# Performance work log

Hardware: AMD Instinct MI355X
Metric: run time of the kernel (lower is better)

The kernel has to match this reference:

```python
import jax, jax.numpy as jnp
import numpy as np

D_MODEL = 1024
N_HEADS = 16
HEAD_DIM = D_MODEL // N_HEADS
SCALE = float(np.sqrt(HEAD_DIM))
NEG_INF = -1e30


def setup_inputs() -> dict:
    key = jax.random.key(0)
    k1, k2, k3 = jax.random.split(key, 3)
    B, S = 4, 2048
    x = jax.random.normal(k1, (B, S, D_MODEL), dtype=jnp.float32)
    attention_mask = jnp.ones((B, S), dtype=jnp.int32)
    # torch Linear(d, 3d, bias=False): y = x @ W^T; store pre-transposed (d, 3d)
    w_qkv = jax.random.normal(k2, (D_MODEL, 3 * D_MODEL), dtype=jnp.float32) * (1.0 / np.sqrt(D_MODEL))
    w_out = jax.random.normal(k3, (D_MODEL, D_MODEL), dtype=jnp.float32) * (1.0 / np.sqrt(D_MODEL))
    return {"x": x, "attention_mask": attention_mask, "w_qkv": w_qkv, "w_out": w_out}


def reference(x, attention_mask, w_qkv, w_out):
    B, S, _ = x.shape
    qkv = jnp.einsum('bsd,de->bse', x, w_qkv)                     # (B,S,3D)
    qkv = qkv.reshape(B, S, 3, N_HEADS, HEAD_DIM)
    q = qkv[:, :, 0].transpose(0, 2, 1, 3)                        # (B,H,S,hd)
    k = qkv[:, :, 1].transpose(0, 2, 1, 3)
    v = qkv[:, :, 2].transpose(0, 2, 1, 3)

    scores = jnp.einsum('bhqd,bhkd->bhqk', q, k) / SCALE          # (B,H,S,S)
    causal_mask = jnp.triu(jnp.ones((S, S), dtype=bool), k=1)     # True above diag
    scores = jnp.where(causal_mask[None, None], NEG_INF, scores)
    pad_mask = (attention_mask == 0)[:, None, None, :]            # (B,1,1,S)
    scores = jnp.where(pad_mask, NEG_INF, scores)

    attn = jax.nn.softmax(scores, axis=-1)                        # dropout=0 (eval)
    out = jnp.einsum('bhqk,bhkd->bhqd', attn, v)                  # (B,H,S,hd)
    out = out.transpose(0, 2, 1, 3).reshape(B, S, D_MODEL)
    return jnp.einsum('bsd,de->bse', out, w_out)
```

## Files before the change

kernel.cpp:

```cpp
#include <hip/hip_runtime.h>


typedef __attribute__((ext_vector_type(8))) short bf16x8;
typedef __attribute__((ext_vector_type(8))) unsigned short u16x8;
typedef __attribute__((ext_vector_type(4))) unsigned short u16x4;
typedef __attribute__((ext_vector_type(4))) float f32x4;

#define MFMA16 __builtin_amdgcn_mfma_f32_16x16x32_bf16

#define GLDS(gp, lp) __builtin_amdgcn_global_load_lds( \
    (const __attribute__((address_space(1))) unsigned int*)(gp), \
    (__attribute__((address_space(3))) unsigned int*)(lp), 16, 0, 0)

__device__ __forceinline__ unsigned short f2bf(float f) {
    union { float f; unsigned int u; } v; v.f = f;
    unsigned int r = v.u + 0x7fffu + ((v.u >> 16) & 1u);
    return (unsigned short)(r >> 16);
}

__global__ void k_prep(const float* __restrict__ x, unsigned short* __restrict__ xb,
                       const int* __restrict__ mask, unsigned short* __restrict__ mb,
                       const float* __restrict__ wqkv, unsigned short* __restrict__ w1t,
                       const float* __restrict__ wout, unsigned short* __restrict__ w2t) {
    __shared__ float tile[32][33];
    const int bx = blockIdx.x;
    if (bx < 4096) {
        size_t i = ((size_t)bx * 256 + threadIdx.x) * 8;
        float4 f0 = *(const float4*)(x + i);
        float4 f1 = *(const float4*)(x + i + 4);
        u16x8 v;
        v[0] = f2bf(f0.x); v[1] = f2bf(f0.y); v[2] = f2bf(f0.z); v[3] = f2bf(f0.w);
        v[4] = f2bf(f1.x); v[5] = f2bf(f1.y); v[6] = f2bf(f1.z); v[7] = f2bf(f1.w);
        *(u16x8*)(xb + i) = v;
        if (bx < 32) {
            int j = bx * 256 + threadIdx.x;
            mb[j] = mask[j] ? (unsigned short)0x3F80 : (unsigned short)0;
        }
    } else {
        const int b2 = bx - 4096;
        const int cb = b2 & 127, rb = b2 >> 7;
        const float* in = (cb < 96) ? wqkv : wout;
        unsigned short* out = (cb < 96) ? w1t : w2t;
        const int C = (cb < 96) ? 3072 : 1024;
        const int c0 = ((cb < 96) ? cb : cb - 96) * 32;
        const int r0 = rb * 32;
        int tx = threadIdx.x & 31, ty = threadIdx.x >> 5;
        for (int i = ty; i < 32; i += 8)
            tile[i][tx] = in[(size_t)(r0 + i) * C + (c0 + tx)];
        __syncthreads();
        for (int i = ty; i < 32; i += 8)
            out[(size_t)(c0 + i) * 1024 + (r0 + tx)] = f2bf(tile[tx][i]);
    }
}

template <int MODE, int NBX>
__global__ __launch_bounds__(512, 2) void k_gemm256(
    const unsigned short* __restrict__ Ab,
    const unsigned short* __restrict__ Bt,
    float* __restrict__ Cf,
    unsigned short* __restrict__ qb,
    unsigned short* __restrict__ kb,
    unsigned short* __restrict__ vt,
    const int* __restrict__ mask,
    int N, int K)
{
    __shared__ __align__(16) unsigned short la[3][128 * 64];
    __shared__ __align__(16) unsigned short lb[3][256 * 64];
    const int t = threadIdx.x;
    const int w = t >> 6, lane = t & 63;
    const int lr = lane & 15, lq = lane >> 4;
    const int lr7 = lr & 7;
    const int rowb = lane >> 3, c8 = lane & 7;
    const int g8 = ((c8 - rowb) & 7) * 8;

    const int nwg = NBX * 64;
    const int orig = blockIdx.y * NBX + blockIdx.x;
    const int rm = (orig & 7) * (nwg >> 3) + (orig >> 3);
    const int m0 = (rm / NBX) * 128;
    const int n0 = (rm % NBX) * 256;

    const int wm = (w >> 2) * 64;
    const int wn = (w & 3) * 64;

    const unsigned short* Arow = Ab + (size_t)(m0 + w * 8 + rowb) * K + g8;
    const unsigned short* Brow = Bt + (size_t)(n0 + w * 8 + rowb) * K + g8;

    auto stage3 = [&](int tt, int g) {
        const int buf = tt % 3;
        const size_t ko = (size_t)tt * 64;
        if (g == 0) {
            GLDS(Arow + ko,                    &la[buf][(w * 8) * 64]);
            GLDS(Brow + ko,                    &lb[buf][(w * 8) * 64]);
            GLDS(Brow + (size_t)64 * K + ko,   &lb[buf][(64 + w * 8) * 64]);
        } else {
            GLDS(Arow + (size_t)64 * K + ko,   &la[buf][(64 + w * 8) * 64]);
            GLDS(Brow + (size_t)128 * K + ko,  &lb[buf][(128 + w * 8) * 64]);
            GLDS(Brow + (size_t)192 * K + ko,  &lb[buf][(192 + w * 8) * 64]);
        }
    };

    f32x4 acc[4][4];
    #pragma unroll
    for (int i = 0; i < 4; ++i)
        #pragma unroll
        for (int j = 0; j < 4; ++j)
            acc[i][j] = (f32x4){0.f, 0.f, 0.f, 0.f};

    const int nt = K >> 6;

    stage3(0, 0); stage3(0, 1); stage3(1, 0); stage3(1, 1);
    asm volatile("s_waitcnt vmcnt(6)" ::: "memory");
    __builtin_amdgcn_sched_barrier(0);
    __builtin_amdgcn_s_barrier();

    for (int tt = 0; tt < nt; ++tt) {
        const unsigned short* lat = la[tt % 3];
        const unsigned short* lbt = lb[tt % 3];
        #pragma unroll
        for (int ks = 0; ks < 2; ++ks) {
            const int pa = ((ks * 4 + lq + lr7) & 7) * 8;
            bf16x8 af[4], bg[4];
            #pragma unroll
            for (int i = 0; i < 4; ++i) {
                af[i] = *(const bf16x8*)&lat[(wm + i * 16 + lr) * 64 + pa];
                bg[i] = *(const bf16x8*)&lbt[(wn + i * 16 + lr) * 64 + pa];
            }
            if (tt + 2 < nt) stage3(tt + 2, ks);
            __builtin_amdgcn_s_barrier();
            __builtin_amdgcn_s_setprio(1);
            #pragma unroll
            for (int i = 0; i < 4; ++i)
                #pragma unroll
                for (int j = 0; j < 4; ++j)
                    acc[i][j] = MFMA16(af[i], bg[j], acc[i][j], 0, 0, 0);
            __builtin_amdgcn_s_setprio(0);
            if (ks == 1) {
                if (tt == nt - 2) {
                    asm volatile("s_waitcnt vmcnt(0)" ::: "memory");
                    __builtin_amdgcn_sched_barrier(0);
                } else if (tt < nt - 2) {
                    asm volatile("s_waitcnt vmcnt(6)" ::: "memory");
                    __builtin_amdgcn_sched_barrier(0);
                }
            }
            __builtin_amdgcn_s_barrier();
        }
    }

    const float QSCALE = 0.18033688f;
    if (MODE == 0) {
        for (int i = 0; i < 4; ++i)
            for (int j = 0; j < 4; ++j)
                for (int r = 0; r < 4; ++r) {
                    int row = m0 + wm + i * 16 + lq * 4 + r;
                    int col = n0 + wn + j * 16 + lr;
                    Cf[(size_t)row * N + col] = acc[i][j][r];
                }
    } else {
        const int which = n0 >> 10;
        if (which < 2) {
            unsigned short* dst = which ? kb : qb;
            const float sc = which ? 1.0f : QSCALE;
            for (int i = 0; i < 4; ++i)
                for (int j = 0; j < 4; ++j)
                    for (int r = 0; r < 4; ++r) {
                        int row = m0 + wm + i * 16 + lq * 4 + r;
                        int col = n0 + wn + j * 16 + lr;
                        int h = (col >> 6) & 15, d = col & 63;
                        int b = row >> 11, s = row & 2047;
                        dst[((size_t)(b * 16 + h) * 2048 + s) * 64 + d] = f2bf(acc[i][j][r] * sc);
                    }
        } else {
            for (int i = 0; i < 4; ++i) {
                int s0 = m0 + wm + i * 16 + lq * 4;
                int b = s0 >> 11, s = s0 & 2047;
                int4 m4 = *(const int4*)&mask[b * 2048 + s];
                for (int j = 0; j < 4; ++j) {
                    int col = n0 + wn + j * 16 + lr;
                    int h = (col >> 6) & 15, d = col & 63;
                    u16x4 pv;
                    pv[0] = m4.x ? f2bf(acc[i][j][0]) : (unsigned short)0;
                    pv[1] = m4.y ? f2bf(acc[i][j][1]) : (unsigned short)0;
                    pv[2] = m4.z ? f2bf(acc[i][j][2]) : (unsigned short)0;
                    pv[3] = m4.w ? f2bf(acc[i][j][3]) : (unsigned short)0;
                    *(u16x4*)&vt[((size_t)(b * 16 + h) * 64 + d) * 2048 + s] = pv;
                }
            }
        }
    }
}

__global__ __launch_bounds__(512, 4) void k_attn(
    const unsigned short* __restrict__ qb,
    const unsigned short* __restrict__ kb,
    const unsigned short* __restrict__ vt,
    const unsigned short* __restrict__ maskbg,
    unsigned short* __restrict__ ao)
{
    __shared__ __align__(16) unsigned short kt_lds[2][64 * 64];
    __shared__ __align__(16) unsigned short vt_lds[2][64 * 64];
    __shared__ __align__(16) unsigned short plds[8][16 * 72];

    const int t = threadIdx.x;
    const int w = t >> 6, lane = t & 63;
    const int lr = lane & 15, lq = lane >> 4;
    const int lr7 = lr & 7;
    const int bh = blockIdx.x, b = bh >> 4, h = bh & 15;

    const unsigned short* qp = qb + (size_t)bh * 2048 * 64;
    const unsigned short* kp = kb + (size_t)bh * 2048 * 64;
    const unsigned short* vp = vt + (size_t)bh * 64 * 2048;
    const unsigned short* mbg = maskbg + b * 2048;
    unsigned short* pw = plds[w];

    const int rowb = lane >> 3, c8 = lane & 7;
    const int sc8 = (c8 ^ rowb) * 8;

    auto stage = [&](int c) {
        const int buf = c & 1;
        const int k0 = c * 64;
        const int rg = 8 * w;
        const int row = rg + rowb;
        GLDS(&kp[(size_t)(k0 + row) * 64 + sc8], &kt_lds[buf][rg * 64]);
        GLDS(&vp[(size_t)row * 2048 + k0 + sc8], &vt_lds[buf][rg * 64]);
    };

    for (int pass = 0; pass < 2; ++pass) {
        const int stripe = pass ? (15 - (int)blockIdx.y) : (int)blockIdx.y;
        const int q0w = stripe * 128 + w * 16;

        bf16x8 aq0 = *(const bf16x8*)&qp[(q0w + lr) * 64 + lq * 8];
        bf16x8 aq1 = *(const bf16x8*)&qp[(q0w + lr) * 64 + 32 + lq * 8];

        f32x4 acc[4], lacc;
        lacc = (f32x4){0.f, 0.f, 0.f, 0.f};
        #pragma unroll
        for (int j = 0; j < 4; ++j) acc[j] = (f32x4){0.f, 0.f, 0.f, 0.f};

        const int nch = 2 * (stripe + 1);
        stage(0);
        for (int c = 0; c < nch; ++c) {
            __syncthreads();
            if (c + 1 < nch) stage(c + 1);
            const int k0 = c * 64;
            if (k0 < q0w + 16) {
                const unsigned short* kt = kt_lds[c & 1];
                const unsigned short* vtl = vt_lds[c & 1];
                const bool causal = (k0 + 63 > q0w);
                const int kcol0 = (lq ^ lr7) * 8;
                const int kcol1 = ((4 + lq) ^ lr7) * 8;
                #pragma unroll
                for (int ki = 0; ki < 4; ++ki) {
                    bf16x8 kf0 = *(const bf16x8*)&kt[(ki * 16 + lr) * 64 + kcol0];
                    bf16x8 kf1 = *(const bf16x8*)&kt[(ki * 16 + lr) * 64 + kcol1];
                    f32x4 s = (f32x4){0.f, 0.f, 0.f, 0.f};
                    s = MFMA16(kf0, aq0, s, 0, 0, 0);
                    s = MFMA16(kf1, aq1, s, 0, 0, 0);
                    unsigned int u[4];
                    #pragma unroll
                    for (int r = 0; r < 4; ++r) {
                        float scv = s[r];
                        if (causal) {
                            int key = k0 + ki * 16 + lq * 4 + r;
                            int qq  = q0w + lr;
                            scv = (key <= qq) ? scv : -3.0e38f;
                        }
                        float p = __builtin_amdgcn_exp2f(scv);
                        union { float f; unsigned int u; } cv; cv.f = p;
                        u[r] = cv.u;
                    }
                    uint2 pk;
                    pk.x = __builtin_amdgcn_perm(u[1], u[0], 0x07060302u);
                    pk.y = __builtin_amdgcn_perm(u[3], u[2], 0x07060302u);
                    *(uint2*)&pw[lr * 72 + ki * 16 + lq * 4] = pk;
                }
                #pragma unroll
                for (int kc = 0; kc < 64; kc += 32) {
                    bf16x8 pf = *(const bf16x8*)&pw[lr * 72 + kc + lq * 8];
                    bf16x8 mb = *(const bf16x8*)&mbg[k0 + kc + lq * 8];
                    const int vcol = (((kc >> 3) + lq) ^ lr7) * 8;
                    #pragma unroll
                    for (int j = 0; j < 4; ++j) {
                        bf16x8 vf = *(const bf16x8*)&vtl[(j * 16 + lr) * 64 + vcol];
                        acc[j] = MFMA16(pf, vf, acc[j], 0, 0, 0);
                    }
                    lacc = MFMA16(pf, mb, lacc, 0, 0, 0);
                }
            }
        }

        #pragma unroll
        for (int r = 0; r < 4; ++r) {
            float inv = 1.0f / fmaxf(lacc[r], 1e-30f);
            int row = q0w + lq * 4 + r;
            #pragma unroll
            for (int j = 0; j < 4; ++j) {
                int d = j * 16 + lr;
                ao[(size_t)(b * 2048 + row) * 1024 + h * 64 + d] = f2bf(acc[j][r] * inv);
            }
        }
        __syncthreads();
    }
}

extern "C" void kernel_launch(void* const* d_in, const int* in_sizes, int n_in,
                              void* d_out, int out_size, void* d_ws, size_t ws_size,
                              hipStream_t stream)
{
    const float* x    = (const float*)d_in[0];
    const int*   mask = (const int*)d_in[1];
    const float* wqkv = (const float*)d_in[2];
    const float* wout = (const float*)d_in[3];
    float* out = (float*)d_out;

    const size_t NEED = ((size_t)8192 * 1024 + (size_t)3072 * 1024 + (size_t)1024 * 1024 +
                         3 * (size_t)64 * 2048 * 64 + (size_t)8192 * 1024 + 8192) * 2;
    if (ws_size < NEED) return;

    char* ws = (char*)d_ws;
    unsigned short* xb  = (unsigned short*)ws; ws += (size_t)8192 * 1024 * 2;
    unsigned short* w1t = (unsigned short*)ws; ws += (size_t)3072 * 1024 * 2;
    unsigned short* w2t = (unsigned short*)ws; ws += (size_t)1024 * 1024 * 2;
    unsigned short* qb  = (unsigned short*)ws; ws += (size_t)64 * 2048 * 64 * 2;
    unsigned short* kb  = (unsigned short*)ws; ws += (size_t)64 * 2048 * 64 * 2;
    unsigned short* vt  = (unsigned short*)ws; ws += (size_t)64 * 64 * 2048 * 2;
    unsigned short* ao  = (unsigned short*)ws; ws += (size_t)8192 * 1024 * 2;
    unsigned short* mbg = (unsigned short*)ws; ws += (size_t)8192 * 2;

    k_prep<<<dim3(8192), 256, 0, stream>>>(x, xb, mask, mbg, wqkv, w1t, wout, w2t);
    k_gemm256<1, 12><<<dim3(12, 64), 512, 0, stream>>>(xb, w1t, nullptr, qb, kb, vt, mask, 3072, 1024);
    k_attn<<<dim3(64, 8), 512, 0, stream>>>(qb, kb, vt, mbg, ao);
    k_gemm256<0, 4><<<dim3(4, 64), 512, 0, stream>>>(ao, w2t, out, nullptr, nullptr, nullptr, nullptr, 1024, 1024);
}
```

Measured before the change: 242.2 us.

## Enlarge GEMM tiles to 256x256 with quadrant-phased double-buffered pipeline

Both projection GEMMs now use 256x256 output tiles instead of 128x256. Each wave computes 128x64 in four quadrant phases, with the next tile's B and A loads interleaved between phases. The buffering drops from triple to double, and the grid is halved. The aim is higher arithmetic intensity per LDS and global byte. In exchange there are twice as many accumulator registers, larger LDS use (likely one block per CU), and fewer workgroups: the QKV GEMM gets 384 blocks and the output GEMM only 128 blocks for 256 CUs.

```diff
diff --git a/kernel.cpp b/kernel.cpp
--- a/kernel.cpp
+++ b/kernel.cpp
@@ -11,6 +11,20 @@
 #define GLDS(gp, lp) __builtin_amdgcn_global_load_lds( \
     (const __attribute__((address_space(1))) unsigned int*)(gp), \
     (__attribute__((address_space(3))) unsigned int*)(lp), 16, 0, 0)
+
+#define PH_GATE() do { \
+    __builtin_amdgcn_sched_barrier(0); \
+    __builtin_amdgcn_s_barrier(); \
+    asm volatile("s_waitcnt lgkmcnt(0)" ::: "memory"); \
+    __builtin_amdgcn_sched_barrier(0); \
+    __builtin_amdgcn_s_setprio(1); \
+} while (0)
+
+#define PH_END() do { \
+    __builtin_amdgcn_s_setprio(0); \
+    __builtin_amdgcn_sched_barrier(0); \
+    __builtin_amdgcn_s_barrier(); \
+} while (0)
 
 __device__ __forceinline__ unsigned short f2bf(float f) {
     union { float f; unsigned int u; } v; v.f = f;
@@ -64,8 +78,8 @@
     const int* __restrict__ mask,
     int N, int K)
 {
-    __shared__ __align__(16) unsigned short la[3][128 * 64];
-    __shared__ __align__(16) unsigned short lb[3][256 * 64];
+    __shared__ __align__(16) unsigned short la[2][256 * 64];
+    __shared__ __align__(16) unsigned short lb[2][256 * 64];
     const int t = threadIdx.x;
     const int w = t >> 6, lane = t & 63;
     const int lr = lane & 15, lq = lane >> 4;
@@ -73,83 +87,133 @@
     const int rowb = lane >> 3, c8 = lane & 7;
     const int g8 = ((c8 - rowb) & 7) * 8;
 
-    const int nwg = NBX * 64;
+    const int nwg = NBX * 32;
     const int orig = blockIdx.y * NBX + blockIdx.x;
     const int rm = (orig & 7) * (nwg >> 3) + (orig >> 3);
-    const int m0 = (rm / NBX) * 128;
+    const int m0 = (rm / NBX) * 256;
     const int n0 = (rm % NBX) * 256;
 
-    const int wm = (w >> 2) * 64;
-    const int wn = (w & 3) * 64;
-
-    const unsigned short* Arow = Ab + (size_t)(m0 + w * 8 + rowb) * K + g8;
-    const unsigned short* Brow = Bt + (size_t)(n0 + w * 8 + rowb) * K + g8;
-
-    auto stage3 = [&](int tt, int g) {
-        const int buf = tt % 3;
-        const size_t ko = (size_t)tt * 64;
-        if (g == 0) {
-            GLDS(Arow + ko,                    &la[buf][(w * 8) * 64]);
-            GLDS(Brow + ko,                    &lb[buf][(w * 8) * 64]);
-            GLDS(Brow + (size_t)64 * K + ko,   &lb[buf][(64 + w * 8) * 64]);
-        } else {
-            GLDS(Arow + (size_t)64 * K + ko,   &la[buf][(64 + w * 8) * 64]);
-            GLDS(Brow + (size_t)128 * K + ko,  &lb[buf][(128 + w * 8) * 64]);
-            GLDS(Brow + (size_t)192 * K + ko,  &lb[buf][(192 + w * 8) * 64]);
-        }
+    const int wr = w >> 2;
+    const int wc = w & 3;
+    const int wm = wr * 128;
+    const int wn = wc * 64;
+
+    auto stageA = [&](int tt2, int hf) {
+        unsigned short* dst = &la[tt2 & 1][(hf * 128 + w * 8) * 64];
+        const unsigned short* src =
+            Ab + (size_t)(m0 + hf * 128 + w * 8 + rowb) * K + (size_t)tt2 * 64 + g8;
+        GLDS(src, dst);
+        GLDS(src + (size_t)64 * K, dst + 64 * 64);
     };
-
-    f32x4 acc[4][4];
+    auto stageB = [&](int tt2, int hf) {
+        unsigned short* dst = &lb[tt2 & 1][(hf * 128 + w * 8) * 64];
+        const unsigned short* src =
+            Bt + (size_t)(n0 + hf * 128 + w * 8 + rowb) * K + (size_t)tt2 * 64 + g8;
+        GLDS(src, dst);
+        GLDS(src + (size_t)64 * K, dst + 64 * 64);
+    };
+
+    f32x4 acc[8][4];
     #pragma unroll
-    for (int i = 0; i < 4; ++i)
+    for (int i = 0; i < 8; ++i)
         #pragma unroll
         for (int j = 0; j < 4; ++j)
             acc[i][j] = (f32x4){0.f, 0.f, 0.f, 0.f};
 
     const int nt = K >> 6;
 
-    stage3(0, 0); stage3(0, 1); stage3(1, 0); stage3(1, 1);
-    asm volatile("s_waitcnt vmcnt(6)" ::: "memory");
+    stageA(0, 0); stageA(0, 1); stageB(0, 0); stageB(0, 1);
+    stageA(1, 0); stageA(1, 1);
+    asm volatile("s_waitcnt vmcnt(4)" ::: "memory");
     __builtin_amdgcn_sched_barrier(0);
     __builtin_amdgcn_s_barrier();
 
     for (int tt = 0; tt < nt; ++tt) {
-        const unsigned short* lat = la[tt % 3];
-        const unsigned short* lbt = lb[tt % 3];
+        const unsigned short* lA = la[tt & 1];
+        const unsigned short* lB = lb[tt & 1];
+        bf16x8 alo[8], ahi[8], blo[4], bhi[4];
+
         #pragma unroll
         for (int ks = 0; ks < 2; ++ks) {
             const int pa = ((ks * 4 + lq + lr7) & 7) * 8;
-            bf16x8 af[4], bg[4];
-            #pragma unroll
-            for (int i = 0; i < 4; ++i) {
-                af[i] = *(const bf16x8*)&lat[(wm + i * 16 + lr) * 64 + pa];
-                bg[i] = *(const bf16x8*)&lbt[(wn + i * 16 + lr) * 64 + pa];
-            }
-            if (tt + 2 < nt) stage3(tt + 2, ks);
-            __builtin_amdgcn_s_barrier();
-            __builtin_amdgcn_s_setprio(1);
-            #pragma unroll
-            for (int i = 0; i < 4; ++i)
-                #pragma unroll
-                for (int j = 0; j < 4; ++j)
-                    acc[i][j] = MFMA16(af[i], bg[j], acc[i][j], 0, 0, 0);
-            __builtin_amdgcn_s_setprio(0);
-            if (ks == 1) {
-                if (tt == nt - 2) {
-                    asm volatile("s_waitcnt vmcnt(0)" ::: "memory");
-                    __builtin_amdgcn_sched_barrier(0);
-                } else if (tt < nt - 2) {
-                    asm volatile("s_waitcnt vmcnt(6)" ::: "memory");
-                    __builtin_amdgcn_sched_barrier(0);
-                }
-            }
-            __builtin_amdgcn_s_barrier();
-        }
+            #pragma unroll
+            for (int i = 0; i < 4; ++i)
+                alo[ks * 4 + i] = *(const bf16x8*)&lA[(wm + i * 16 + lr) * 64 + pa];
+            #pragma unroll
+            for (int j = 0; j < 2; ++j)
+                blo[ks * 2 + j] = *(const bf16x8*)&lB[(wn + j * 16 + lr) * 64 + pa];
+        }
+        if (tt + 1 < nt) stageB(tt + 1, 0);
+        PH_GATE();
+        #pragma unroll
+        for (int ks = 0; ks < 2; ++ks)
+            #pragma unroll
+            for (int i = 0; i < 4; ++i)
+                #pragma unroll
+                for (int j = 0; j < 2; ++j)
+                    acc[i][j] = MFMA16(alo[ks * 4 + i], blo[ks * 2 + j], acc[i][j], 0, 0, 0);
+        PH_END();
+
+        #pragma unroll
+        for (int ks = 0; ks < 2; ++ks) {
+            const int pa = ((ks * 4 + lq + lr7) & 7) * 8;
+            #pragma unroll
+            for (int i = 0; i < 4; ++i)
+                ahi[ks * 4 + i] = *(const bf16x8*)&lA[(wm + 64 + i * 16 + lr) * 64 + pa];
+        }
+        if (tt + 1 < nt) stageB(tt + 1, 1);
+        PH_GATE();
+        #pragma unroll
+        for (int ks = 0; ks < 2; ++ks)
+            #pragma unroll
+            for (int i = 0; i < 4; ++i)
+                #pragma unroll
+                for (int j = 0; j < 2; ++j)
+                    acc[4 + i][j] = MFMA16(ahi[ks * 4 + i], blo[ks * 2 + j], acc[4 + i][j], 0, 0, 0);
+        PH_END();
+
+        #pragma unroll
+        for (int ks = 0; ks < 2; ++ks) {
+            const int pa = ((ks * 4 + lq + lr7) & 7) * 8;
+            #pragma unroll
+            for (int j = 0; j < 2; ++j)
+                bhi[ks * 2 + j] = *(const bf16x8*)&lB[(wn + 32 + j * 16 + lr) * 64 + pa];
+        }
+        if (tt + 2 < nt) stageA(tt + 2, 0);
+        PH_GATE();
+        #pragma unroll
+        for (int ks = 0; ks < 2; ++ks)
+            #pragma unroll
+            for (int i = 0; i < 4; ++i)
+                #pragma unroll
+                for (int j = 0; j < 2; ++j)
+                    acc[i][2 + j] = MFMA16(alo[ks * 4 + i], bhi[ks * 2 + j], acc[i][2 + j], 0, 0, 0);
+        PH_END();
+
+        if (tt + 2 < nt) stageA(tt + 2, 1);
+        __builtin_amdgcn_sched_barrier(0);
+        __builtin_amdgcn_s_barrier();
+        __builtin_amdgcn_s_setprio(1);
+        #pragma unroll
+        for (int ks = 0; ks < 2; ++ks)
+            #pragma unroll
+            for (int i = 0; i < 4; ++i)
+                #pragma unroll
+                for (int j = 0; j < 2; ++j)
+                    acc[4 + i][2 + j] = MFMA16(ahi[ks * 4 + i], bhi[ks * 2 + j], acc[4 + i][2 + j], 0, 0, 0);
+        __builtin_amdgcn_s_setprio(0);
+        if (tt < nt - 2) {
+            asm volatile("s_waitcnt vmcnt(4)" ::: "memory");
+        } else if (tt == nt - 2) {
+            asm volatile("s_waitcnt vmcnt(0)" ::: "memory");
+        }
+        __builtin_amdgcn_sched_barrier(0);
+        __builtin_amdgcn_s_barrier();
     }
 
     const float QSCALE = 0.18033688f;
     if (MODE == 0) {
-        for (int i = 0; i < 4; ++i)
+        for (int i = 0; i < 8; ++i)
             for (int j = 0; j < 4; ++j)
                 for (int r = 0; r < 4; ++r) {
                     int row = m0 + wm + i * 16 + lq * 4 + r;
@@ -161,7 +225,7 @@
         if (which < 2) {
             unsigned short* dst = which ? kb : qb;
             const float sc = which ? 1.0f : QSCALE;
-            for (int i = 0; i < 4; ++i)
+            for (int i = 0; i < 8; ++i)
                 for (int j = 0; j < 4; ++j)
                     for (int r = 0; r < 4; ++r) {
                         int row = m0 + wm + i * 16 + lq * 4 + r;
@@ -171,7 +235,7 @@
                         dst[((size_t)(b * 16 + h) * 2048 + s) * 64 + d] = f2bf(acc[i][j][r] * sc);
                     }
         } else {
-            for (int i = 0; i < 4; ++i) {
+            for (int i = 0; i < 8; ++i) {
                 int s0 = m0 + wm + i * 16 + lq * 4;
                 int b = s0 >> 11, s = s0 & 2047;
                 int4 m4 = *(const int4*)&mask[b * 2048 + s];
@@ -328,7 +392,7 @@
     unsigned short* mbg = (unsigned short*)ws; ws += (size_t)8192 * 2;
 
     k_prep<<<dim3(8192), 256, 0, stream>>>(x, xb, mask, mbg, wqkv, w1t, wout, w2t);
-    k_gemm256<1, 12><<<dim3(12, 64), 512, 0, stream>>>(xb, w1t, nullptr, qb, kb, vt, mask, 3072, 1024);
+    k_gemm256<1, 12><<<dim3(12, 32), 512, 0, stream>>>(xb, w1t, nullptr, qb, kb, vt, mask, 3072, 1024);
     k_attn<<<dim3(64, 8), 512, 0, stream>>>(qb, kb, vt, mbg, ao);
-    k_gemm256<0, 4><<<dim3(4, 64), 512, 0, stream>>>(ao, w2t, out, nullptr, nullptr, nullptr, nullptr, 1024, 1024);
-}
+    k_gemm256<0, 4><<<dim3(4, 32), 512, 0, stream>>>(ao, w2t, out, nullptr, nullptr, nullptr, nullptr, 1024, 1024);
+}
```

Result: slower. 256.6 us (+6.0%).
